# Kernel tuning notes

Measured on AMD Instinct MI355X. Metric: run time of the kernel, lower is better.

## Reference

```python
import jax, jax.numpy as jnp
from jax import lax
import numpy as np

NUM_POINTS = 2048  # init_kwargs: num_points
BIG = 1e10


def setup_inputs() -> dict:
    key = jax.random.key(0)
    points = jax.random.normal(key, (16, 3, 32768), dtype=jnp.float32)
    return {"points": points}


def furthest_point_sampling(xyz, m):
    """xyz: [B, N, 3]. Returns indices [B, m] (int32), first index = 0 (CUDA FPS convention)."""
    B, N, _ = xyz.shape

    def step(carry, _):
        dist, last_idx = carry                                   # [B,N], [B]
        last_pt = jnp.take_along_axis(xyz, last_idx[:, None, None], axis=1)  # [B,1,3]
        d = jnp.sum((xyz - last_pt) ** 2, axis=-1)               # [B,N]
        dist = jnp.minimum(dist, d)
        nxt = jnp.argmax(dist, axis=1).astype(jnp.int32)         # [B]
        return (dist, nxt), last_idx                             # emit current selection

    init = (jnp.full((B, N), BIG, dtype=xyz.dtype), jnp.zeros((B,), jnp.int32))
    _, idxs = lax.scan(step, init, None, length=m)               # [m, B]
    return idxs.T                                                # [B, m]


def fps_gather_by_index(points, idx):
    """points: [B, C, N]; idx: [B, m] -> [B, C, m]."""
    return jnp.take_along_axis(points, idx[:, None, :], axis=2)


def reference(points):
    xyz = jnp.transpose(points, (0, 2, 1))          # [B, N, 3]
    ind = furthest_point_sampling(xyz, NUM_POINTS)  # [B, M]
    return fps_gather_by_index(points, ind)         # [B, 3, M]
```

## Files before the change

kernel.cpp:

```cpp
#include <hip/hip_runtime.h>

#define FPS_N 32768
#define FPS_M 2048
#define FPS_B 16
#define BLK_PER_B 8
#define FPS_T 576
#define SCT 512
#define PTS (FPS_N / BLK_PER_B)
#define PPT (PTS / SCT)
#define KPUB 4
#define RING 128
#define WSTRIDE 320

typedef unsigned long long ull;

#define DPP_MAX_STEP(ctrl, rmask)                                              \
    {                                                                          \
        unsigned plo = (unsigned)__builtin_amdgcn_update_dpp(                  \
            (int)lo, (int)lo, (ctrl), (rmask), 0xf, false);                    \
        unsigned phi = (unsigned)__builtin_amdgcn_update_dpp(                  \
            (int)hi, (int)hi, (ctrl), (rmask), 0xf, false);                    \
        if (phi > hi || (phi == hi && plo > lo)) { hi = phi; lo = plo; }       \
    }

__device__ __forceinline__ ull wave_max_u64(ull v) {
    unsigned lo = (unsigned)v, hi = (unsigned)(v >> 32);
    DPP_MAX_STEP(0x111, 0xf)
    DPP_MAX_STEP(0x112, 0xf)
    DPP_MAX_STEP(0x114, 0xf)
    DPP_MAX_STEP(0x118, 0xf)
    DPP_MAX_STEP(0x142, 0xa)
    DPP_MAX_STEP(0x143, 0xc)
    unsigned blo = (unsigned)__builtin_amdgcn_readlane((int)lo, 63);
    unsigned bhi = (unsigned)__builtin_amdgcn_readlane((int)hi, 63);
    return ((ull)bhi << 32) | blo;
}

__device__ __forceinline__ unsigned wave_max_bits(unsigned v) {
    int m = (int)v;
#define DPP_IMAX_STEP(ctrl)                                                    \
    {                                                                          \
        int p = __builtin_amdgcn_update_dpp((int)m, (int)m, (ctrl), 0xf, 0xf,  \
                                            false);                            \
        m = p > m ? p : m;                                                     \
    }
    DPP_IMAX_STEP(0x111)
    DPP_IMAX_STEP(0x112)
    DPP_IMAX_STEP(0x114)
    DPP_IMAX_STEP(0x118)
    int r0 = __builtin_amdgcn_readlane(m, 15);
    int r1 = __builtin_amdgcn_readlane(m, 31);
    int r2 = __builtin_amdgcn_readlane(m, 47);
    int r3 = __builtin_amdgcn_readlane(m, 63);
    int a = r0 > r1 ? r0 : r1;
    int b = r2 > r3 ? r2 : r3;
    return (unsigned)(a > b ? a : b);
}

__device__ __forceinline__ unsigned wave_min_u32(unsigned v) {
    unsigned m = v;
#define DPP_UMIN_STEP(ctrl, rmask)                                             \
    {                                                                          \
        unsigned p = (unsigned)__builtin_amdgcn_update_dpp(                    \
            (int)m, (int)m, (ctrl), (rmask), 0xf, false);                      \
        if (p < m) m = p;                                                      \
    }
    DPP_UMIN_STEP(0x111, 0xf)
    DPP_UMIN_STEP(0x112, 0xf)
    DPP_UMIN_STEP(0x114, 0xf)
    DPP_UMIN_STEP(0x118, 0xf)
    DPP_UMIN_STEP(0x142, 0xa)
    DPP_UMIN_STEP(0x143, 0xc)
    return (unsigned)__builtin_amdgcn_readlane((int)m, 63);
}

__device__ __forceinline__ float readlane_f(float v, int l) {
    return __uint_as_float(
        (unsigned)__builtin_amdgcn_readlane((int)__float_as_uint(v), l));
}

__global__ __launch_bounds__(FPS_T)
__attribute__((amdgpu_waves_per_eu(1)))
void fps_kernel(const float* __restrict__ pts, float* __restrict__ out,
                ull* __restrict__ ws) {
#pragma clang fp contract(off)
    __shared__ float srx[RING], sry[RING], srz[RING];
    __shared__ unsigned rtag[RING];
    __shared__ unsigned etot;

    const int blk = blockIdx.x;
    const int b = blk & 15;
    const int j = blk >> 4;
    const int tid = threadIdx.x;
    const int lane = tid & 63;
    const float* __restrict__ X = pts + (size_t)b * 3 * FPS_N;
    const float* __restrict__ Y = X + FPS_N;
    const float* __restrict__ Z = Y + FPS_N;
    const int off = j * PTS;
    float* __restrict__ outb = out + (size_t)b * 3 * FPS_M;
    ull* __restrict__ wsb = ws + (size_t)b * WSTRIDE;

    for (int q = tid; q < RING; q += FPS_T) rtag[q] = 0;
    if (tid == 0) etot = 0;
    __syncthreads();

    const float p0x = X[0], p0y = Y[0], p0z = Z[0];

    if (tid < 64) {
        if (j == 0 && lane == 0) {
            outb[0] = p0x; outb[FPS_M] = p0y; outb[2 * FPS_M] = p0z;
        }
        int last = 0;
        for (unsigned e = 1; last < FPS_M - 1; ++e) {
            ull cv[KPUB];
            float ccx[KPUB], ccy[KPUB], ccz[KPUB];
#pragma unroll
            for (int c = 0; c < KPUB; ++c) {
                cv[c] = 0; ccx[c] = 0.0f; ccy[c] = 0.0f; ccz[c] = 0.0f;
            }
            unsigned kcm = 0;
            bool kw = false;
            ull cw = 0;
            for (int it = 0; it < (1 << 25); ++it) {
                ull pv[KPUB + 1];
#pragma unroll
                for (int c = 0; c < KPUB; ++c)
                    pv[c] = (kcm & (1u << c))
                                ? 0
                                : __hip_atomic_load(wsb + c * 64 + lane,
                                                    __ATOMIC_RELAXED,
                                                    __HIP_MEMORY_SCOPE_AGENT);
                if (!kw)
                    pv[KPUB] = __hip_atomic_load(wsb + 256 + lane,
                                                 __ATOMIC_RELAXED,
                                                 __HIP_MEMORY_SCOPE_AGENT);
#pragma unroll
                for (int c = 0; c < KPUB; ++c) {
                    if (!(kcm & (1u << c)) &&
                        (unsigned)(pv[c] & 0xFFFull) == e) {
                        cv[c] = pv[c];
                        kcm |= 1u << c;
                        const int g = 32767 - (int)((pv[c] >> 17) & 0x7FFFull);
                        ccx[c] = X[g];
                        ccy[c] = Y[g];
                        ccz[c] = Z[g];
                    }
                }
                if (!kw) {
                    cw = pv[KPUB];
                    kw = ((unsigned)(cw & 0xFFFull) == e);
                }
                if (__all((kcm == ((1u << KPUB) - 1)) && kw)) break;
                __builtin_amdgcn_s_sleep(1);
            }
            const ull vcutg = wave_max_u64(cw);
            int posted = 0;
            while (last < FPS_M - 1 && posted < RING) {
                ull m = cv[0];
#pragma unroll
                for (int c = 1; c < KPUB; ++c)
                    if (cv[c] > m) m = cv[c];
                const unsigned mhi = (unsigned)(m >> 32);
                const unsigned Whi = wave_max_bits(mhi);
                const ull tb = __ballot(mhi == Whi);
                ull W;
                if (__popcll(tb) == 1) {
                    const int wl0 = (int)(__ffsll((long long)tb) - 1);
                    const unsigned wlo = (unsigned)__builtin_amdgcn_readlane(
                        (int)(unsigned)(m & 0xFFFFFFFFull), wl0);
                    W = ((ull)Whi << 32) | wlo;
                } else {
                    W = wave_max_u64(m);
                }
                if (W <= vcutg) break;
                bool own = false;
                float sx = 0.0f, sy = 0.0f, sz = 0.0f;
#pragma unroll
                for (int c = 0; c < KPUB; ++c) {
                    const bool h = (cv[c] == W);
                    own |= h;
                    sx = h ? ccx[c] : sx;
                    sy = h ? ccy[c] : sy;
                    sz = h ? ccz[c] : sz;
                    cv[c] = h ? 0 : cv[c];
                }
                const ull mk = __ballot(own);
                const int wl = __ffsll((long long)mk) - 1;
                const float wx = readlane_f(sx, wl);
                const float wy = readlane_f(sy, wl);
                const float wz = readlane_f(sz, wl);
#pragma unroll
                for (int c = 0; c < KPUB; ++c) {
                    float dx = ccx[c] - wx, dy = ccy[c] - wy, dz = ccz[c] - wz;
                    float d = (dx * dx + dy * dy) + dz * dz;
                    float df = __uint_as_float((unsigned)(cv[c] >> 32));
                    float nd = d < df ? d : df;
                    cv[c] = ((ull)__float_as_uint(nd) << 32)
                          | (cv[c] & 0xFFFFFFFFull);
                }
                ++last; ++posted;
                const int slot = last & (RING - 1);
                if (lane == 0) {
                    srx[slot] = wx; sry[slot] = wy; srz[slot] = wz;
                    __hip_atomic_store(&rtag[slot], (unsigned)last,
                                       __ATOMIC_RELEASE,
                                       __HIP_MEMORY_SCOPE_WORKGROUP);
                }
            }
            if (lane == 0)
                __hip_atomic_store(&etot, (e << 16) | (unsigned)last,
                                   __ATOMIC_RELAXED, __HIP_MEMORY_SCOPE_WORKGROUP);
        }
    } else {
        const int st = tid - 64;
        const int w = (tid >> 6) - 1;
        const int wid = j * 8 + w;
        float cx[PPT], cy[PPT], cz[PPT], dist[PPT];
#pragma unroll
        for (int k = 0; k < PPT; ++k) {
            const int g = off + k * SCT + st;
            cx[k] = X[g]; cy[k] = Y[g]; cz[k] = Z[g];
            float dx = cx[k] - p0x, dy = cy[k] - p0y, dz = cz[k] - p0z;
            dist[k] = (dx * dx + dy * dy) + dz * dz;
        }
        const int goff = off + st;
        unsigned applied = 0;
        for (unsigned e = 1;; ++e) {
            float fd[PPT];
#pragma unroll
            for (int k = 0; k < PPT; ++k) fd[k] = dist[k];
            for (int r = 0; r < KPUB + 1; ++r) {
                float m = fd[0];
#pragma unroll
                for (int k = 1; k < PPT; ++k) m = fmaxf(m, fd[k]);
                const unsigned Wb = wave_max_bits(__float_as_uint(m));
                unsigned mg = 0xFFFFFFFFu;
#pragma unroll
                for (int k = PPT - 1; k >= 0; --k)
                    if (__float_as_uint(fd[k]) == Wb)
                        mg = (unsigned)(goff + k * SCT);
                const ull mk = __ballot(mg != 0xFFFFFFFFu);
                unsigned gw;
                if (__popcll(mk) == 1) {
                    gw = (unsigned)__builtin_amdgcn_readlane(
                        (int)mg, (int)(__ffsll((long long)mk) - 1));
                } else {
                    gw = wave_min_u32(mg);
                }
                const ull word = ((ull)Wb << 32)
                               | ((ull)(32767u - gw) << 17) | (ull)e;
                if (r < KPUB) {
#pragma unroll
                    for (int k = 0; k < PPT; ++k)
                        if ((unsigned)(goff + k * SCT) == gw)
                            fd[k] = -1.0f;
                    if (lane == r)
                        __hip_atomic_store(wsb + r * 64 + wid, word,
                                           __ATOMIC_RELAXED,
                                           __HIP_MEMORY_SCOPE_AGENT);
                } else {
                    if (lane == KPUB)
                        __hip_atomic_store(wsb + 256 + wid, word,
                                           __ATOMIC_RELAXED,
                                           __HIP_MEMORY_SCOPE_AGENT);
                }
            }
            unsigned last_row = 0;
            bool have = false;
            for (;;) {
                bool did = false;
                if (!have) {
                    unsigned u = __hip_atomic_load(&etot, __ATOMIC_RELAXED,
                                                   __HIP_MEMORY_SCOPE_WORKGROUP);
                    if ((u >> 16) == e) { last_row = u & 0xFFFFu; have = true; did = true; }
                }
                const unsigned want = applied + 1;
                if (!have || want <= last_row) {
                    const int slot = (int)(want & (RING - 1));
                    if (__hip_atomic_load(&rtag[slot], __ATOMIC_ACQUIRE,
                                          __HIP_MEMORY_SCOPE_WORKGROUP) == want) {
                        const float wx = srx[slot], wy = sry[slot], wz = srz[slot];
#pragma unroll
                        for (int k = 0; k < PPT; ++k) {
                            float dx = cx[k] - wx, dy = cy[k] - wy, dz = cz[k] - wz;
                            float d = (dx * dx + dy * dy) + dz * dz;
                            dist[k] = d < dist[k] ? d : dist[k];
                        }
                        if (j == 0 && w == 0 && lane < 3) {
                            float cvv = lane == 0 ? wx : (lane == 1 ? wy : wz);
                            outb[(size_t)lane * FPS_M + want] = cvv;
                        }
                        applied = want;
                        did = true;
                    }
                }
                if (have && applied == last_row) break;
                if (!did) __builtin_amdgcn_s_sleep(1);
            }
            if (last_row >= FPS_M - 1) break;
        }
    }
}

extern "C" void kernel_launch(void* const* d_in, const int* in_sizes, int n_in,
                              void* d_out, int out_size, void* d_ws, size_t ws_size,
                              hipStream_t stream) {
    const float* pts = (const float*)d_in[0];
    float* out = (float*)d_out;
    ull* ws = (ull*)d_ws;
    void* args[] = { (void*)&pts, (void*)&out, (void*)&ws };
    hipLaunchCooperativeKernel((const void*)fps_kernel,
                               dim3(FPS_B * BLK_PER_B), dim3(FPS_T),
                               args, 0, stream);
}
```

Measured before the change: 1.157 ms.

## Replace dedicated selector wave and LDS ring with per-wave redundant selection

Result: slower. 1.688 ms (+45.9%).

```diff
diff --git a/kernel.cpp b/kernel.cpp
--- a/kernel.cpp
+++ b/kernel.cpp
@@ -4,13 +4,11 @@
 #define FPS_M 2048
 #define FPS_B 16
 #define BLK_PER_B 8
-#define FPS_T 576
-#define SCT 512
+#define FPS_T 512
 #define PTS (FPS_N / BLK_PER_B)
-#define PPT (PTS / SCT)
+#define PPT (PTS / FPS_T)
 #define KPUB 4
-#define RING 128
-#define WSTRIDE 320
+#define WSTRIDE 640
 
 typedef unsigned long long ull;
 
@@ -53,8 +51,8 @@
     int r2 = __builtin_amdgcn_readlane(m, 47);
     int r3 = __builtin_amdgcn_readlane(m, 63);
     int a = r0 > r1 ? r0 : r1;
-    int b = r2 > r3 ? r2 : r3;
-    return (unsigned)(a > b ? a : b);
+    int bq = r2 > r3 ? r2 : r3;
+    return (unsigned)(a > bq ? a : bq);
 }
 
 __device__ __forceinline__ unsigned wave_min_u32(unsigned v) {
@@ -84,220 +82,174 @@
 void fps_kernel(const float* __restrict__ pts, float* __restrict__ out,
                 ull* __restrict__ ws) {
 #pragma clang fp contract(off)
-    __shared__ float srx[RING], sry[RING], srz[RING];
-    __shared__ unsigned rtag[RING];
-    __shared__ unsigned etot;
-
     const int blk = blockIdx.x;
     const int b = blk & 15;
     const int j = blk >> 4;
     const int tid = threadIdx.x;
     const int lane = tid & 63;
+    const int w = tid >> 6;
+    const int wid = j * 8 + w;
     const float* __restrict__ X = pts + (size_t)b * 3 * FPS_N;
     const float* __restrict__ Y = X + FPS_N;
     const float* __restrict__ Z = Y + FPS_N;
     const int off = j * PTS;
     float* __restrict__ outb = out + (size_t)b * 3 * FPS_M;
     ull* __restrict__ wsb = ws + (size_t)b * WSTRIDE;
-
-    for (int q = tid; q < RING; q += FPS_T) rtag[q] = 0;
-    if (tid == 0) etot = 0;
-    __syncthreads();
+    const bool emitter = (wid == 0);
 
     const float p0x = X[0], p0y = Y[0], p0z = Z[0];
-
-    if (tid < 64) {
-        if (j == 0 && lane == 0) {
-            outb[0] = p0x; outb[FPS_M] = p0y; outb[2 * FPS_M] = p0z;
-        }
-        int last = 0;
-        for (unsigned e = 1; last < FPS_M - 1; ++e) {
-            ull cv[KPUB];
-            float ccx[KPUB], ccy[KPUB], ccz[KPUB];
+    if (emitter && lane == 0) {
+        outb[0] = p0x; outb[FPS_M] = p0y; outb[2 * FPS_M] = p0z;
+    }
+
+    float cx[PPT], cy[PPT], cz[PPT], dist[PPT];
+#pragma unroll
+    for (int k = 0; k < PPT; ++k) {
+        const int g = off + k * FPS_T + tid;
+        cx[k] = X[g]; cy[k] = Y[g]; cz[k] = Z[g];
+        float dx = cx[k] - p0x, dy = cy[k] - p0y, dz = cz[k] - p0z;
+        dist[k] = (dx * dx + dy * dy) + dz * dz;
+    }
+    const int goff = off + tid;
+
+    int last = 0;
+    for (unsigned e = 1; last < FPS_M - 1; ++e) {
+        ull* const grp = wsb + (e & 1) * 320;
+        float fd[PPT];
+#pragma unroll
+        for (int k = 0; k < PPT; ++k) fd[k] = dist[k];
+        for (int r = 0; r < KPUB + 1; ++r) {
+            float m = fd[0];
+#pragma unroll
+            for (int k = 1; k < PPT; ++k) m = fmaxf(m, fd[k]);
+            const unsigned Wb = wave_max_bits(__float_as_uint(m));
+            unsigned mg = 0xFFFFFFFFu;
+#pragma unroll
+            for (int k = PPT - 1; k >= 0; --k)
+                if (__float_as_uint(fd[k]) == Wb)
+                    mg = (unsigned)(goff + k * FPS_T);
+            const ull mk = __ballot(mg != 0xFFFFFFFFu);
+            unsigned gw;
+            if (__popcll(mk) == 1) {
+                gw = (unsigned)__builtin_amdgcn_readlane(
+                    (int)mg, (int)(__ffsll((long long)mk) - 1));
+            } else {
+                gw = wave_min_u32(mg);
+            }
+            const ull word = ((ull)Wb << 32)
+                           | ((ull)(32767u - gw) << 17) | (ull)e;
+            if (r < KPUB) {
+#pragma unroll
+                for (int k = 0; k < PPT; ++k)
+                    if ((unsigned)(goff + k * FPS_T) == gw)
+                        fd[k] = -1.0f;
+                if (lane == r)
+                    __hip_atomic_store(grp + r * 64 + wid, word,
+                                       __ATOMIC_RELAXED,
+                                       __HIP_MEMORY_SCOPE_AGENT);
+            } else {
+                if (lane == KPUB)
+                    __hip_atomic_store(grp + 256 + wid, word,
+                                       __ATOMIC_RELAXED,
+                                       __HIP_MEMORY_SCOPE_AGENT);
+            }
+        }
+        ull cv[KPUB];
+        float ccx[KPUB], ccy[KPUB], ccz[KPUB];
+#pragma unroll
+        for (int c = 0; c < KPUB; ++c) {
+            cv[c] = 0; ccx[c] = 0.0f; ccy[c] = 0.0f; ccz[c] = 0.0f;
+        }
+        unsigned kcm = 0;
+        bool kw = false;
+        ull cw = 0;
+        for (int it = 0; it < (1 << 25); ++it) {
+            ull pv[KPUB + 1];
+#pragma unroll
+            for (int c = 0; c < KPUB; ++c)
+                pv[c] = (kcm & (1u << c))
+                            ? 0
+                            : __hip_atomic_load(grp + c * 64 + lane,
+                                                __ATOMIC_RELAXED,
+                                                __HIP_MEMORY_SCOPE_AGENT);
+            if (!kw)
+                pv[KPUB] = __hip_atomic_load(grp + 256 + lane,
+                                             __ATOMIC_RELAXED,
+                                             __HIP_MEMORY_SCOPE_AGENT);
 #pragma unroll
             for (int c = 0; c < KPUB; ++c) {
-                cv[c] = 0; ccx[c] = 0.0f; ccy[c] = 0.0f; ccz[c] = 0.0f;
-            }
-            unsigned kcm = 0;
-            bool kw = false;
-            ull cw = 0;
-            for (int it = 0; it < (1 << 25); ++it) {
-                ull pv[KPUB + 1];
-#pragma unroll
-                for (int c = 0; c < KPUB; ++c)
-                    pv[c] = (kcm & (1u << c))
-                                ? 0
-                                : __hip_atomic_load(wsb + c * 64 + lane,
-                                                    __ATOMIC_RELAXED,
-                                                    __HIP_MEMORY_SCOPE_AGENT);
-                if (!kw)
-                    pv[KPUB] = __hip_atomic_load(wsb + 256 + lane,
-                                                 __ATOMIC_RELAXED,
-                                                 __HIP_MEMORY_SCOPE_AGENT);
-#pragma unroll
-                for (int c = 0; c < KPUB; ++c) {
-                    if (!(kcm & (1u << c)) &&
-                        (unsigned)(pv[c] & 0xFFFull) == e) {
-                        cv[c] = pv[c];
-                        kcm |= 1u << c;
-                        const int g = 32767 - (int)((pv[c] >> 17) & 0x7FFFull);
-                        ccx[c] = X[g];
-                        ccy[c] = Y[g];
-                        ccz[c] = Z[g];
-                    }
+                if (!(kcm & (1u << c)) &&
+                    (unsigned)(pv[c] & 0xFFFull) == e) {
+                    cv[c] = pv[c];
+                    kcm |= 1u << c;
+                    const int g = 32767 - (int)((pv[c] >> 17) & 0x7FFFull);
+                    ccx[c] = X[g];
+                    ccy[c] = Y[g];
+                    ccz[c] = Z[g];
                 }
-                if (!kw) {
-                    cw = pv[KPUB];
-                    kw = ((unsigned)(cw & 0xFFFull) == e);
-                }
-                if (__all((kcm == ((1u << KPUB) - 1)) && kw)) break;
-                __builtin_amdgcn_s_sleep(1);
-            }
-            const ull vcutg = wave_max_u64(cw);
-            int posted = 0;
-            while (last < FPS_M - 1 && posted < RING) {
-                ull m = cv[0];
-#pragma unroll
-                for (int c = 1; c < KPUB; ++c)
-                    if (cv[c] > m) m = cv[c];
-                const unsigned mhi = (unsigned)(m >> 32);
-                const unsigned Whi = wave_max_bits(mhi);
-                const ull tb = __ballot(mhi == Whi);
-                ull W;
-                if (__popcll(tb) == 1) {
-                    const int wl0 = (int)(__ffsll((long long)tb) - 1);
-                    const unsigned wlo = (unsigned)__builtin_amdgcn_readlane(
-                        (int)(unsigned)(m & 0xFFFFFFFFull), wl0);
-                    W = ((ull)Whi << 32) | wlo;
-                } else {
-                    W = wave_max_u64(m);
-                }
-                if (W <= vcutg) break;
-                bool own = false;
-                float sx = 0.0f, sy = 0.0f, sz = 0.0f;
-#pragma unroll
-                for (int c = 0; c < KPUB; ++c) {
-                    const bool h = (cv[c] == W);
-                    own |= h;
-                    sx = h ? ccx[c] : sx;
-                    sy = h ? ccy[c] : sy;
-                    sz = h ? ccz[c] : sz;
-                    cv[c] = h ? 0 : cv[c];
-                }
-                const ull mk = __ballot(own);
-                const int wl = __ffsll((long long)mk) - 1;
-                const float wx = readlane_f(sx, wl);
-                const float wy = readlane_f(sy, wl);
-                const float wz = readlane_f(sz, wl);
-#pragma unroll
-                for (int c = 0; c < KPUB; ++c) {
-                    float dx = ccx[c] - wx, dy = ccy[c] - wy, dz = ccz[c] - wz;
-                    float d = (dx * dx + dy * dy) + dz * dz;
-                    float df = __uint_as_float((unsigned)(cv[c] >> 32));
-                    float nd = d < df ? d : df;
-                    cv[c] = ((ull)__float_as_uint(nd) << 32)
-                          | (cv[c] & 0xFFFFFFFFull);
-                }
-                ++last; ++posted;
-                const int slot = last & (RING - 1);
-                if (lane == 0) {
-                    srx[slot] = wx; sry[slot] = wy; srz[slot] = wz;
-                    __hip_atomic_store(&rtag[slot], (unsigned)last,
-                                       __ATOMIC_RELEASE,
-                                       __HIP_MEMORY_SCOPE_WORKGROUP);
-                }
-            }
-            if (lane == 0)
-                __hip_atomic_store(&etot, (e << 16) | (unsigned)last,
-                                   __ATOMIC_RELAXED, __HIP_MEMORY_SCOPE_WORKGROUP);
-        }
-    } else {
-        const int st = tid - 64;
-        const int w = (tid >> 6) - 1;
-        const int wid = j * 8 + w;
-        float cx[PPT], cy[PPT], cz[PPT], dist[PPT];
-#pragma unroll
-        for (int k = 0; k < PPT; ++k) {
-            const int g = off + k * SCT + st;
-            cx[k] = X[g]; cy[k] = Y[g]; cz[k] = Z[g];
-            float dx = cx[k] - p0x, dy = cy[k] - p0y, dz = cz[k] - p0z;
-            dist[k] = (dx * dx + dy * dy) + dz * dz;
-        }
-        const int goff = off + st;
-        unsigned applied = 0;
-        for (unsigned e = 1;; ++e) {
-            float fd[PPT];
-#pragma unroll
-            for (int k = 0; k < PPT; ++k) fd[k] = dist[k];
-            for (int r = 0; r < KPUB + 1; ++r) {
-                float m = fd[0];
-#pragma unroll
-                for (int k = 1; k < PPT; ++k) m = fmaxf(m, fd[k]);
-                const unsigned Wb = wave_max_bits(__float_as_uint(m));
-                unsigned mg = 0xFFFFFFFFu;
-#pragma unroll
-                for (int k = PPT - 1; k >= 0; --k)
-                    if (__float_as_uint(fd[k]) == Wb)
-                        mg = (unsigned)(goff + k * SCT);
-                const ull mk = __ballot(mg != 0xFFFFFFFFu);
-                unsigned gw;
-                if (__popcll(mk) == 1) {
-                    gw = (unsigned)__builtin_amdgcn_readlane(
-                        (int)mg, (int)(__ffsll((long long)mk) - 1));
-                } else {
-                    gw = wave_min_u32(mg);
-                }
-                const ull word = ((ull)Wb << 32)
-                               | ((ull)(32767u - gw) << 17) | (ull)e;
-                if (r < KPUB) {
-#pragma unroll
-                    for (int k = 0; k < PPT; ++k)
-                        if ((unsigned)(goff + k * SCT) == gw)
-                            fd[k] = -1.0f;
-                    if (lane == r)
-                        __hip_atomic_store(wsb + r * 64 + wid, word,
-                                           __ATOMIC_RELAXED,
-                                           __HIP_MEMORY_SCOPE_AGENT);
-                } else {
-                    if (lane == KPUB)
-                        __hip_atomic_store(wsb + 256 + wid, word,
-                                           __ATOMIC_RELAXED,
-                                           __HIP_MEMORY_SCOPE_AGENT);
-                }
-            }
-            unsigned last_row = 0;
-            bool have = false;
-            for (;;) {
-                bool did = false;
-                if (!have) {
-                    unsigned u = __hip_atomic_load(&etot, __ATOMIC_RELAXED,
-                                                   __HIP_MEMORY_SCOPE_WORKGROUP);
-                    if ((u >> 16) == e) { last_row = u & 0xFFFFu; have = true; did = true; }
-                }
-                const unsigned want = applied + 1;
-                if (!have || want <= last_row) {
-                    const int slot = (int)(want & (RING - 1));
-                    if (__hip_atomic_load(&rtag[slot], __ATOMIC_ACQUIRE,
-                                          __HIP_MEMORY_SCOPE_WORKGROUP) == want) {
-                        const float wx = srx[slot], wy = sry[slot], wz = srz[slot];
-#pragma unroll
-                        for (int k = 0; k < PPT; ++k) {
-                            float dx = cx[k] - wx, dy = cy[k] - wy, dz = cz[k] - wz;
-                            float d = (dx * dx + dy * dy) + dz * dz;
-                            dist[k] = d < dist[k] ? d : dist[k];
-                        }
-                        if (j == 0 && w == 0 && lane < 3) {
-                            float cvv = lane == 0 ? wx : (lane == 1 ? wy : wz);
-                            outb[(size_t)lane * FPS_M + want] = cvv;
-                        }
-                        applied = want;
-                        did = true;
-                    }
-                }
-                if (have && applied == last_row) break;
-                if (!did) __builtin_amdgcn_s_sleep(1);
-            }
-            if (last_row >= FPS_M - 1) break;
+            }
+            if (!kw) {
+                cw = pv[KPUB];
+                kw = ((unsigned)(cw & 0xFFFull) == e);
+            }
+            if (__all((kcm == ((1u << KPUB) - 1)) && kw)) break;
+            __builtin_amdgcn_s_sleep(1);
+        }
+        const ull vcutg = wave_max_u64(cw);
+        while (last < FPS_M - 1) {
+            ull m = cv[0];
+#pragma unroll
+            for (int c = 1; c < KPUB; ++c)
+                if (cv[c] > m) m = cv[c];
+            const unsigned mhi = (unsigned)(m >> 32);
+            const unsigned Whi = wave_max_bits(mhi);
+            const ull tb = __ballot(mhi == Whi);
+            ull W;
+            if (__popcll(tb) == 1) {
+                const int wl0 = (int)(__ffsll((long long)tb) - 1);
+                const unsigned wlo = (unsigned)__builtin_amdgcn_readlane(
+                    (int)(unsigned)(m & 0xFFFFFFFFull), wl0);
+                W = ((ull)Whi << 32) | wlo;
+            } else {
+                W = wave_max_u64(m);
+            }
+            if (W <= vcutg) break;
+            bool own = false;
+            float sx = 0.0f, sy = 0.0f, sz = 0.0f;
+#pragma unroll
+            for (int c = 0; c < KPUB; ++c) {
+                const bool h = (cv[c] == W);
+                own |= h;
+                sx = h ? ccx[c] : sx;
+                sy = h ? ccy[c] : sy;
+                sz = h ? ccz[c] : sz;
+                cv[c] = h ? 0 : cv[c];
+            }
+            const ull mk = __ballot(own);
+            const int wl = __ffsll((long long)mk) - 1;
+            const float wx = readlane_f(sx, wl);
+            const float wy = readlane_f(sy, wl);
+            const float wz = readlane_f(sz, wl);
+#pragma unroll
+            for (int c = 0; c < KPUB; ++c) {
+                float dx = ccx[c] - wx, dy = ccy[c] - wy, dz = ccz[c] - wz;
+                float d = (dx * dx + dy * dy) + dz * dz;
+                float df = __uint_as_float((unsigned)(cv[c] >> 32));
+                float nd = d < df ? d : df;
+                cv[c] = ((ull)__float_as_uint(nd) << 32)
+                      | (cv[c] & 0xFFFFFFFFull);
+            }
+            ++last;
+#pragma unroll
+            for (int k = 0; k < PPT; ++k) {
+                float dx = cx[k] - wx, dy = cy[k] - wy, dz = cz[k] - wz;
+                float d = (dx * dx + dy * dy) + dz * dz;
+                dist[k] = d < dist[k] ? d : dist[k];
+            }
+            if (emitter && lane < 3) {
+                float cvv = lane == 0 ? wx : (lane == 1 ? wy : wz);
+                outb[(size_t)lane * FPS_M + last] = cvv;
+            }
         }
     }
 }
```

## Poll a cache-coherent mirror of candidate slots and double-buffer workspace by epoch parity

Applied to the files above, without the earlier changes.

New measurement: 1.124 ms, median of 3. 1.03x faster.

```diff
diff --git a/kernel.cpp b/kernel.cpp
--- a/kernel.cpp
+++ b/kernel.cpp
@@ -10,7 +10,7 @@
 #define PPT (PTS / SCT)
 #define KPUB 4
 #define RING 128
-#define WSTRIDE 320
+#define WSTRIDE 960
 
 typedef unsigned long long ull;
 
@@ -53,8 +53,8 @@
     int r2 = __builtin_amdgcn_readlane(m, 47);
     int r3 = __builtin_amdgcn_readlane(m, 63);
     int a = r0 > r1 ? r0 : r1;
-    int b = r2 > r3 ? r2 : r3;
-    return (unsigned)(a > b ? a : b);
+    int bq = r2 > r3 ? r2 : r3;
+    return (unsigned)(a > bq ? a : bq);
 }
 
 __device__ __forceinline__ unsigned wave_min_u32(unsigned v) {
@@ -99,6 +99,7 @@
     const int off = j * PTS;
     float* __restrict__ outb = out + (size_t)b * 3 * FPS_M;
     ull* __restrict__ wsb = ws + (size_t)b * WSTRIDE;
+    ull* __restrict__ mir = wsb + 640;
 
     for (int q = tid; q < RING; q += FPS_T) rtag[q] = 0;
     if (tid == 0) etot = 0;
@@ -110,8 +111,14 @@
         if (j == 0 && lane == 0) {
             outb[0] = p0x; outb[FPS_M] = p0y; outb[2 * FPS_M] = p0z;
         }
+        const ull ma0 = (ull)(uintptr_t)(mir + 0 * 64 + lane);
+        const ull ma1 = (ull)(uintptr_t)(mir + 1 * 64 + lane);
+        const ull ma2 = (ull)(uintptr_t)(mir + 2 * 64 + lane);
+        const ull ma3 = (ull)(uintptr_t)(mir + 3 * 64 + lane);
+        const ull mac = (ull)(uintptr_t)(mir + 256 + lane);
         int last = 0;
         for (unsigned e = 1; last < FPS_M - 1; ++e) {
+            ull* const grp = wsb + (e & 1) * 320;
             ull cv[KPUB];
             float ccx[KPUB], ccy[KPUB], ccz[KPUB];
 #pragma unroll
@@ -122,18 +129,18 @@
             bool kw = false;
             ull cw = 0;
             for (int it = 0; it < (1 << 25); ++it) {
-                ull pv[KPUB + 1];
-#pragma unroll
-                for (int c = 0; c < KPUB; ++c)
-                    pv[c] = (kcm & (1u << c))
-                                ? 0
-                                : __hip_atomic_load(wsb + c * 64 + lane,
-                                                    __ATOMIC_RELAXED,
-                                                    __HIP_MEMORY_SCOPE_AGENT);
-                if (!kw)
-                    pv[KPUB] = __hip_atomic_load(wsb + 256 + lane,
-                                                 __ATOMIC_RELAXED,
-                                                 __HIP_MEMORY_SCOPE_AGENT);
+                ull q0, q1, q2, q3, q4;
+                asm volatile(
+                    "global_load_dwordx2 %0, %5, off sc0\n\t"
+                    "global_load_dwordx2 %1, %6, off sc0\n\t"
+                    "global_load_dwordx2 %2, %7, off sc0\n\t"
+                    "global_load_dwordx2 %3, %8, off sc0\n\t"
+                    "global_load_dwordx2 %4, %9, off sc0\n\t"
+                    "s_waitcnt vmcnt(0)"
+                    : "=&v"(q0), "=&v"(q1), "=&v"(q2), "=&v"(q3), "=&v"(q4)
+                    : "v"(ma0), "v"(ma1), "v"(ma2), "v"(ma3), "v"(mac)
+                    : "memory");
+                ull pv[KPUB + 1] = {q0, q1, q2, q3, q4};
 #pragma unroll
                 for (int c = 0; c < KPUB; ++c) {
                     if (!(kcm & (1u << c)) &&
@@ -146,11 +153,42 @@
                         ccz[c] = Z[g];
                     }
                 }
-                if (!kw) {
-                    cw = pv[KPUB];
-                    kw = ((unsigned)(cw & 0xFFFull) == e);
-                }
-                if (__all((kcm == ((1u << KPUB) - 1)) && kw)) break;
+                if (!kw && (unsigned)(pv[KPUB] & 0xFFFull) == e) {
+                    cw = pv[KPUB]; kw = true;
+                }
+                bool done = __all((kcm == ((1u << KPUB) - 1)) && kw);
+                if (!done) {
+                    ull av[KPUB + 1];
+#pragma unroll
+                    for (int c = 0; c < KPUB; ++c)
+                        av[c] = (kcm & (1u << c))
+                                    ? 0
+                                    : __hip_atomic_load(grp + c * 64 + lane,
+                                                        __ATOMIC_RELAXED,
+                                                        __HIP_MEMORY_SCOPE_AGENT);
+                    av[KPUB] = kw ? 0
+                                  : __hip_atomic_load(grp + 256 + lane,
+                                                      __ATOMIC_RELAXED,
+                                                      __HIP_MEMORY_SCOPE_AGENT);
+#pragma unroll
+                    for (int c = 0; c < KPUB; ++c) {
+                        if (!(kcm & (1u << c)) &&
+                            (unsigned)(av[c] & 0xFFFull) == e) {
+                            cv[c] = av[c];
+                            kcm |= 1u << c;
+                            const int g =
+                                32767 - (int)((av[c] >> 17) & 0x7FFFull);
+                            ccx[c] = X[g];
+                            ccy[c] = Y[g];
+                            ccz[c] = Z[g];
+                        }
+                    }
+                    if (!kw && (unsigned)(av[KPUB] & 0xFFFull) == e) {
+                        cw = av[KPUB]; kw = true;
+                    }
+                    done = __all((kcm == ((1u << KPUB) - 1)) && kw);
+                }
+                if (done) break;
                 __builtin_amdgcn_s_sleep(1);
             }
             const ull vcutg = wave_max_u64(cw);
@@ -226,6 +264,7 @@
         const int goff = off + st;
         unsigned applied = 0;
         for (unsigned e = 1;; ++e) {
+            ull* const grp = wsb + (e & 1) * 320;
             float fd[PPT];
 #pragma unroll
             for (int k = 0; k < PPT; ++k) fd[k] = dist[k];
@@ -254,15 +293,23 @@
                     for (int k = 0; k < PPT; ++k)
                         if ((unsigned)(goff + k * SCT) == gw)
                             fd[k] = -1.0f;
-                    if (lane == r)
-                        __hip_atomic_store(wsb + r * 64 + wid, word,
+                    if (lane == r) {
+                        __hip_atomic_store(mir + r * 64 + wid, word,
+                                           __ATOMIC_RELAXED,
+                                           __HIP_MEMORY_SCOPE_WORKGROUP);
+                        __hip_atomic_store(grp + r * 64 + wid, word,
                                            __ATOMIC_RELAXED,
                                            __HIP_MEMORY_SCOPE_AGENT);
+                    }
                 } else {
-                    if (lane == KPUB)
-                        __hip_atomic_store(wsb + 256 + wid, word,
+                    if (lane == KPUB) {
+                        __hip_atomic_store(mir + 256 + wid, word,
+                                           __ATOMIC_RELAXED,
+                                           __HIP_MEMORY_SCOPE_WORKGROUP);
+                        __hip_atomic_store(grp + 256 + wid, word,
                                            __ATOMIC_RELAXED,
                                            __HIP_MEMORY_SCOPE_AGENT);
+                    }
                 }
             }
             unsigned last_row = 0;
```
